# Optimization experiments

Hardware: AMD Instinct MI355X
Metric: run time of the kernel (lower is better)

Reference implementation:

```python
import jax, jax.numpy as jnp
import numpy as np
import math

B, S, D, H, R = 4, 2048, 512, 8, 8  # R = k+1 relative slots per direction


def setup_inputs() -> dict:
    key = jax.random.key(0)
    ks = jax.random.split(key, 16)
    dk = D // H
    sc = 1.0 / math.sqrt(D)
    return {
        "query": jax.random.normal(ks[0], (B, S, D), jnp.float32),
        "key": jax.random.normal(ks[1], (B, S, D), jnp.float32),
        "value": jax.random.normal(ks[2], (B, S, D), jnp.float32),
        "start_nodes": jax.random.randint(ks[3], (B, H, R, S), 0, S, jnp.int64 if jax.config.jax_enable_x64 else jnp.int32),
        "end_nodes": jax.random.randint(ks[4], (B, H, R, S), 0, S, jnp.int64 if jax.config.jax_enable_x64 else jnp.int32),
        "rel_q": jax.random.normal(ks[5], (1, H, 2 * R, dk), jnp.float32),
        "rel_k": jax.random.normal(ks[6], (1, H, 2 * R, dk), jnp.float32),
        "rel_v": jax.random.normal(ks[7], (1, H, 2 * R, dk), jnp.float32),
        "Wq": jax.random.normal(ks[8], (D, D), jnp.float32) * sc,
        "bq": jnp.zeros((D,), jnp.float32),
        "Wk": jax.random.normal(ks[9], (D, D), jnp.float32) * sc,
        "bk": jnp.zeros((D,), jnp.float32),
        "Wv": jax.random.normal(ks[10], (D, D), jnp.float32) * sc,
        "bv": jnp.zeros((D,), jnp.float32),
        "Wo": jax.random.normal(ks[11], (D, D), jnp.float32) * sc,
        "bo": jnp.zeros((D,), jnp.float32),
    }


def reference(query, key, value, start_nodes, end_nodes, rel_q, rel_k, rel_v,
              Wq, bq, Wk, bk, Wv, bv, Wo, bo):
    Bs, Ss, Ds = query.shape
    Hs = start_nodes.shape[1]
    dk = Ds // Hs

    def proj(x, W, b):
        return (x @ W.T + b).reshape(Bs, Ss, Hs, dk).transpose(0, 2, 1, 3)  # [B,H,S,dk]

    q = proj(query, Wq, bq)
    k = proj(key, Wk, bk)
    v = proj(value, Wv, bv)

    start_mask = start_nodes == -1
    sn = jnp.where(start_mask, 0, start_nodes)  # -1 padding -> 0 (masked out below)
    qidx = jnp.concatenate([end_nodes, sn], axis=2)  # [B,H,2R,S]
    kidx = jnp.concatenate([sn, end_nodes], axis=2)

    bi = jnp.arange(Bs)[:, None, None, None]
    hi = jnp.arange(Hs)[None, :, None, None]
    q_ctx = q[bi, hi, qidx]  # [B,H,2R,S,dk]
    k_ctx = k[bi, hi, kidx]
    v_ctx = v[bi, hi, kidx]

    # c2c + c2p + p2c, scale_factor = 3 (rel_q and rel_k both provided)
    scores = ((q_ctx * k_ctx).sum(-1)
              + (q_ctx * rel_k[:, :, :, None, :]).sum(-1)
              + (rel_q[:, :, :, None, :] * k_ctx).sum(-1))
    scores = scores / (3.0 * jnp.sqrt(jnp.asarray(dk, scores.dtype)))

    # mask: padded edges masked in both halves; first S flat entries always masked
    mask = jnp.concatenate([start_mask, start_mask], axis=2).reshape(Bs, Hs, -1)
    mask = mask.at[:, :, :Ss].set(True)
    sflat = jnp.exp(jnp.where(mask, -1e9, scores.reshape(Bs, Hs, -1)))  # [B,H,2R*S]

    qf = qidx.reshape(Bs, Hs, -1)
    b2 = jnp.arange(Bs)[:, None, None]
    h2 = jnp.arange(Hs)[None, :, None]
    # scatter-add softmax denominator over destination nodes, then gather back
    denom = jnp.zeros((Bs, Hs, Ss), sflat.dtype).at[b2, h2, qf].add(sflat)
    denom = jnp.where(denom == 0, -1e9, denom)
    probs = (sflat / denom[b2, h2, qf]).reshape(Bs, Hs, -1, Ss, 1)  # [B,H,2R,S,1]

    attn_v = probs * (v_ctx + rel_v[:, :, :, None, :])  # [B,H,2R,S,dk]
    out = jnp.zeros((Bs, Hs, Ss, dk), attn_v.dtype).at[b2, h2, qf].add(
        attn_v.reshape(Bs, Hs, -1, dk))  # scatter-add aggregation over edges

    out = out.transpose(0, 2, 1, 3).reshape(Bs, Ss, Ds)
    return out @ Wo.T + bo
```

## Files before the change

### kernel.cpp

```cpp
#include <hip/hip_runtime.h>
#include <math.h>

#define B_ 4
#define S_ 2048
#define D_ 512
#define H_ 8
#define R_ 8
#define DK_ 64
#define EPB   (2*R_*S_)
#define ELLCAP 64

typedef __attribute__((ext_vector_type(8))) short bf16x8;
typedef __attribute__((ext_vector_type(8))) unsigned short ushort8_t;
typedef __attribute__((ext_vector_type(4))) float f32x4;

__device__ inline unsigned short f2bf(float f) {
    unsigned u = __builtin_bit_cast(unsigned, f);
    u += 0x7fffu + ((u >> 16) & 1u);
    return (unsigned short)(u >> 16);
}
__device__ inline float bf2f(unsigned short u) {
    return __builtin_bit_cast(float, ((unsigned)u) << 16);
}

__global__ __launch_bounds__(256) void prep(
    const float* __restrict__ query, const float* __restrict__ key,
    const float* __restrict__ value,
    const float* __restrict__ Wq, const float* __restrict__ Wk,
    const float* __restrict__ Wv, const float* __restrict__ Wo,
    const float* __restrict__ rel_q, const float* __restrict__ rel_k,
    const float* __restrict__ rel_v,
    unsigned short* __restrict__ aq, unsigned short* __restrict__ ak,
    unsigned short* __restrict__ av,
    unsigned short* __restrict__ wqp, unsigned short* __restrict__ wkp,
    unsigned short* __restrict__ wvp, unsigned short* __restrict__ wop,
    unsigned short* __restrict__ rqb, unsigned short* __restrict__ rkb,
    unsigned short* __restrict__ rvb)
{
    int bid = blockIdx.x;
    int t = threadIdx.x;
    if (bid < 6656) {
        const float* x;
        unsigned short* y;
        int fi;
        if (bid < 6144) {
            int z = bid >> 11;
            x = (z == 0) ? query : (z == 1) ? key : value;
            y = (z == 0) ? aq : (z == 1) ? ak : av;
            fi = (bid & 2047) * 256 + t;
        } else {
            int r = bid - 6144;
            int z = r >> 7;
            x = (z == 0) ? Wq : (z == 1) ? Wk : (z == 2) ? Wv : Wo;
            y = (z == 0) ? wqp : (z == 1) ? wkp : (z == 2) ? wvp : wop;
            fi = (r & 127) * 256 + t;
        }
        int lane = fi & 63;
        int mg   = fi >> 10;
        int kc   = (fi >> 6) & 15;
        int row  = mg * 16 + (lane & 15);
        int col  = kc * 32 + ((lane >> 4) << 3);
        const float* src = x + (size_t)row * D_ + col;
        float4 a0 = *(const float4*)src;
        float4 a1 = *(const float4*)(src + 4);
        ushort8_t c;
        c[0] = f2bf(a0.x); c[1] = f2bf(a0.y); c[2] = f2bf(a0.z); c[3] = f2bf(a0.w);
        c[4] = f2bf(a1.x); c[5] = f2bf(a1.y); c[6] = f2bf(a1.z); c[7] = f2bf(a1.w);
        *(ushort8_t*)&y[(size_t)fi * 8] = c;
    } else {
        int rr = bid - 6656;
        int z = rr >> 3;
        const float* x = (z == 0) ? rel_q : (z == 1) ? rel_k : rel_v;
        unsigned short* y = (z == 0) ? rqb : (z == 1) ? rkb : rvb;
        size_t i = ((size_t)(rr & 7) * 256 + t) * 4;
        float4 v = *(const float4*)&x[i];
        *(ushort4*)&y[i] = make_ushort4(f2bf(v.x), f2bf(v.y), f2bf(v.z), f2bf(v.w));
    }
}

__global__ __launch_bounds__(256) void gemm_qkv(
    const unsigned short* __restrict__ A0, const unsigned short* __restrict__ A1,
    const unsigned short* __restrict__ A2,
    const unsigned short* __restrict__ W0, const unsigned short* __restrict__ W1,
    const unsigned short* __restrict__ W2,
    const float* __restrict__ bi0, const float* __restrict__ bi1, const float* __restrict__ bi2,
    unsigned short* __restrict__ C0, unsigned short* __restrict__ C1,
    unsigned short* __restrict__ C2)
{
    const int bi  = blockIdx.x;
    const int xcd = bi & 7;
    const int r   = bi >> 3;
    const int z   = r >> 5;
    const int rr  = r & 31;
    const int mg0 = (xcd * 8 + (rr >> 2)) * 8;
    const int ng0 = (rr & 3) * 8;

    const unsigned short* A = (z == 0) ? A0 : (z == 1) ? A1 : A2;
    const unsigned short* W = (z == 0) ? W0 : (z == 1) ? W1 : W2;
    const float* bias       = (z == 0) ? bi0 : (z == 1) ? bi1 : bi2;
    unsigned short* C       = (z == 0) ? C0 : (z == 1) ? C1 : C2;

    const int t    = threadIdx.x;
    const int lane = t & 63;
    const int w    = t >> 6;
    const int wm   = w >> 1, wn = w & 1;

    f32x4 acc[4][4] = {};

    #pragma unroll 2
    for (int kc = 0; kc < 16; ++kc) {
        bf16x8 af[4], bfr[4];
        #pragma unroll
        for (int fm = 0; fm < 4; ++fm) {
            int mg = mg0 + wm * 4 + fm;
            af[fm] = *(const bf16x8*)&A[(size_t)(((mg * 16 + kc) << 6) + lane) * 8];
        }
        #pragma unroll
        for (int fn = 0; fn < 4; ++fn) {
            int ng = ng0 + wn * 4 + fn;
            bfr[fn] = *(const bf16x8*)&W[(size_t)(((ng * 16 + kc) << 6) + lane) * 8];
        }
        #pragma unroll
        for (int fm = 0; fm < 4; ++fm)
            #pragma unroll
            for (int fn = 0; fn < 4; ++fn)
                acc[fm][fn] = __builtin_amdgcn_mfma_f32_16x16x32_bf16(af[fm], bfr[fn], acc[fm][fn], 0, 0, 0);
    }

    #pragma unroll
    for (int fm = 0; fm < 4; ++fm) {
        #pragma unroll
        for (int fn = 0; fn < 4; ++fn) {
            #pragma unroll
            for (int rg = 0; rg < 4; ++rg) {
                int m = (mg0 + wm * 4 + fm) * 16 + (lane >> 4) * 4 + rg;
                int n = (ng0 + wn * 4 + fn) * 16 + (lane & 15);
                float val = acc[fm][fn][rg] + bias[n];
                int b = m >> 11, s = m & (S_ - 1);
                int h = n >> 6,  d = n & 63;
                C[((((size_t)b * H_ + h) * S_ + s) << 6) + d] = f2bf(val);
            }
        }
    }
}

__global__ __launch_bounds__(256) void gemm_out(
    const unsigned short* __restrict__ A, const unsigned short* __restrict__ W,
    const float* __restrict__ bias, float* __restrict__ Cf)
{
    const int bi  = blockIdx.x;
    const int xcd = bi & 7;
    const int r   = bi >> 3;
    const int mg0 = (xcd * 8 + (r >> 3)) * 8;
    const int ng0 = (r & 7) * 4;

    const int t    = threadIdx.x;
    const int lane = t & 63;
    const int w    = t >> 6;
    const int wm   = w >> 1, wn = w & 1;

    f32x4 acc[4][2] = {};

    #pragma unroll 2
    for (int kc = 0; kc < 16; ++kc) {
        bf16x8 af[4], bfr[2];
        #pragma unroll
        for (int fm = 0; fm < 4; ++fm) {
            int mg = mg0 + wm * 4 + fm;
            af[fm] = *(const bf16x8*)&A[(size_t)(((mg * 16 + kc) << 6) + lane) * 8];
        }
        #pragma unroll
        for (int fn = 0; fn < 2; ++fn) {
            int ng = ng0 + wn * 2 + fn;
            bfr[fn] = *(const bf16x8*)&W[(size_t)(((ng * 16 + kc) << 6) + lane) * 8];
        }
        #pragma unroll
        for (int fm = 0; fm < 4; ++fm)
            #pragma unroll
            for (int fn = 0; fn < 2; ++fn)
                acc[fm][fn] = __builtin_amdgcn_mfma_f32_16x16x32_bf16(af[fm], bfr[fn], acc[fm][fn], 0, 0, 0);
    }

    #pragma unroll
    for (int fm = 0; fm < 4; ++fm) {
        #pragma unroll
        for (int fn = 0; fn < 2; ++fn) {
            #pragma unroll
            for (int rg = 0; rg < 4; ++rg) {
                int m = (mg0 + wm * 4 + fm) * 16 + (lane >> 4) * 4 + rg;
                int n = (ng0 + wn * 2 + fn) * 16 + (lane & 15);
                Cf[(size_t)m * D_ + n] = acc[fm][fn][rg] + bias[n];
            }
        }
    }
}

__global__ __launch_bounds__(1024) void attn_fused(
    const unsigned short* __restrict__ q, const unsigned short* __restrict__ k_,
    const unsigned short* __restrict__ v_,
    const unsigned short* __restrict__ rel_q, const unsigned short* __restrict__ rel_k,
    const unsigned short* __restrict__ rel_v,
    const int* __restrict__ start_nodes, const int* __restrict__ end_nodes,
    unsigned short* __restrict__ attn)
{
    __shared__ unsigned short ell[128 * ELLCAP];
    __shared__ int cnt[128];
    const int bi  = blockIdx.x;
    const int xcd = bi & 7;
    const int loc = bi >> 3;
    const int bh  = xcd * 4 + (loc >> 4);
    const int dlo = (loc & 15) << 7;
    const int t   = threadIdx.x;

    if (t < 128) cnt[t] = 0;
    __syncthreads();

    const int base_idx = bh * (R_ * S_);
    for (int f = t; f < EPB; f += 1024) {
        int r2 = f >> 11;
        if (r2 == 0) continue;
        int s = f & (S_ - 1);
        int idx = base_idx + (r2 & 7) * S_ + s;
        int sn = start_nodes[idx];
        if (sn == -1) continue;
        int en = end_nodes[idx];
        int dst = (r2 < R_) ? en : sn;
        unsigned rel = (unsigned)(dst - dlo);
        if (rel < 128u) {
            int ki = (r2 < R_) ? sn : en;
            int pos = atomicAdd(&cnt[rel], 1);
            if (pos < ELLCAP)
                ell[(rel << 6) + pos] = (unsigned short)((r2 << 11) | ki);
        }
    }
    __syncthreads();

    const int w    = t >> 6;
    const int lane = t & 63;
    const int grp  = lane >> 3;
    const int sub  = lane & 7;
    const int h    = bh & 7;
    const size_t node_base = ((size_t)bh << 11);

    for (int dd = 0; dd < 8; ++dd) {
        int dl  = dd * 16 + w;
        int dst = dlo + dl;

        ushort8_t q8 = *(const ushort8_t*)&q[((node_base + dst) << 6) + sub * 8];
        float qv[8];
        #pragma unroll
        for (int i = 0; i < 8; ++i) qv[i] = bf2f(q8[i]);

        int n = cnt[dl];
        if (n > ELLCAP) n = ELLCAP;
        int d_all = (int)ell[(dl << 6) + lane];

        float den = 0.f;
        float o[8] = {};
        #pragma unroll 2
        for (int j = 0; j < n; j += 8) {
            int slot = j + grp;
            int d = __shfl(d_all, slot);
            bool valid = slot < n;
            int ki = d & (S_ - 1);
            int r2 = (d >> 11) & 15;
            ushort8_t k8  = *(const ushort8_t*)&k_  [((node_base + ki) << 6) + sub * 8];
            ushort8_t rk8 = *(const ushort8_t*)&rel_k[(((h << 4) + r2) << 6) + sub * 8];
            ushort8_t rq8 = *(const ushort8_t*)&rel_q[(((h << 4) + r2) << 6) + sub * 8];
            float p = 0.f;
            #pragma unroll
            for (int i = 0; i < 8; ++i)
                p = fmaf(bf2f(k8[i]), qv[i] + bf2f(rq8[i]),
                         fmaf(qv[i], bf2f(rk8[i]), p));
            p += __shfl_xor(p, 1);
            p += __shfl_xor(p, 2);
            p += __shfl_xor(p, 4);
            float sf = valid ? __expf(p * (1.0f / 24.0f)) : 0.f;
            ushort8_t v8  = *(const ushort8_t*)&v_  [((node_base + ki) << 6) + sub * 8];
            ushort8_t rv8 = *(const ushort8_t*)&rel_v[(((h << 4) + r2) << 6) + sub * 8];
            den += sf;
            #pragma unroll
            for (int i = 0; i < 8; ++i)
                o[i] = fmaf(sf, bf2f(v8[i]) + bf2f(rv8[i]), o[i]);
        }
        den += __shfl_xor(den, 8); den += __shfl_xor(den, 16); den += __shfl_xor(den, 32);
        #pragma unroll
        for (int i = 0; i < 8; ++i) {
            o[i] += __shfl_xor(o[i], 8);
            o[i] += __shfl_xor(o[i], 16);
            o[i] += __shfl_xor(o[i], 32);
        }
        if (grp == 0) {
            float inv = (den > 0.f) ? 1.0f / den : 0.f;
            ushort8_t rs;
            #pragma unroll
            for (int i = 0; i < 8; ++i) rs[i] = f2bf(o[i] * inv);
            int m  = ((bh >> 3) << 11) + dst;
            int kc = (h << 1) + (sub >> 2);
            int ln = (m & 15) + ((sub & 3) << 4);
            *(ushort8_t*)&attn[(size_t)((((m >> 4) * 16 + kc) << 6) + ln) * 8] = rs;
        }
    }
}

extern "C" void kernel_launch(void* const* d_in, const int* in_sizes, int n_in,
                              void* d_out, int out_size, void* d_ws, size_t ws_size,
                              hipStream_t stream) {
    const float* query = (const float*)d_in[0];
    const float* key   = (const float*)d_in[1];
    const float* value = (const float*)d_in[2];
    const int* start_nodes = (const int*)d_in[3];
    const int* end_nodes   = (const int*)d_in[4];
    const float* rel_q = (const float*)d_in[5];
    const float* rel_k = (const float*)d_in[6];
    const float* rel_v = (const float*)d_in[7];
    const float* Wq = (const float*)d_in[8];
    const float* bq = (const float*)d_in[9];
    const float* Wk = (const float*)d_in[10];
    const float* bk = (const float*)d_in[11];
    const float* Wv = (const float*)d_in[12];
    const float* bv = (const float*)d_in[13];
    const float* Wo = (const float*)d_in[14];
    const float* bo = (const float*)d_in[15];
    float* out = (float*)d_out;

    const size_t NQ = (size_t)B_ * H_ * S_ * DK_;
    const size_t NW = (size_t)D_ * D_;
    const size_t NR = (size_t)H_ * 2 * R_ * DK_;
    unsigned short* p = (unsigned short*)d_ws;
    unsigned short* aq = p;            p += NQ;
    unsigned short* ak = p;            p += NQ;
    unsigned short* av = p;            p += NQ;
    unsigned short* q  = p;            p += NQ;
    unsigned short* k  = p;            p += NQ;
    unsigned short* v  = p;            p += NQ;
    unsigned short* attn = p;          p += NQ;
    unsigned short* wqp = p;           p += NW;
    unsigned short* wkp = p;           p += NW;
    unsigned short* wvp = p;           p += NW;
    unsigned short* wop = p;           p += NW;
    unsigned short* rqb = p;           p += NR;
    unsigned short* rkb = p;           p += NR;
    unsigned short* rvb = p;           p += NR;

    prep<<<6680, 256, 0, stream>>>(query, key, value, Wq, Wk, Wv, Wo,
                                   rel_q, rel_k, rel_v,
                                   aq, ak, av, wqp, wkp, wvp, wop,
                                   rqb, rkb, rvb);

    gemm_qkv<<<768, 256, 0, stream>>>(aq, ak, av, wqp, wkp, wvp,
                                      bq, bk, bv, q, k, v);

    attn_fused<<<512, 1024, 0, stream>>>(q, k, v, rqb, rkb, rvb,
                                         start_nodes, end_nodes, attn);

    gemm_out<<<512, 256, 0, stream>>>(attn, wop, bo, out);
}
```

Baseline: 226.1 us.

## Fuse fp32-to-bf16 conversion into QKV GEMM with LDS-staged swizzled tiles

```diff
diff --git a/kernel.cpp b/kernel.cpp
--- a/kernel.cpp
+++ b/kernel.cpp
@@ -23,119 +23,130 @@
     return __builtin_bit_cast(float, ((unsigned)u) << 16);
 }
 
-__global__ __launch_bounds__(256) void prep(
-    const float* __restrict__ query, const float* __restrict__ key,
-    const float* __restrict__ value,
-    const float* __restrict__ Wq, const float* __restrict__ Wk,
-    const float* __restrict__ Wv, const float* __restrict__ Wo,
+__global__ __launch_bounds__(256) void gemm_qkv_fused(
+    const float* __restrict__ A0, const float* __restrict__ A1,
+    const float* __restrict__ A2,
+    const float* __restrict__ W0, const float* __restrict__ W1,
+    const float* __restrict__ W2, const float* __restrict__ Wo,
+    const float* __restrict__ bi0, const float* __restrict__ bi1, const float* __restrict__ bi2,
     const float* __restrict__ rel_q, const float* __restrict__ rel_k,
     const float* __restrict__ rel_v,
-    unsigned short* __restrict__ aq, unsigned short* __restrict__ ak,
-    unsigned short* __restrict__ av,
-    unsigned short* __restrict__ wqp, unsigned short* __restrict__ wkp,
-    unsigned short* __restrict__ wvp, unsigned short* __restrict__ wop,
+    unsigned short* __restrict__ C0, unsigned short* __restrict__ C1,
+    unsigned short* __restrict__ C2,
+    unsigned short* __restrict__ wop,
     unsigned short* __restrict__ rqb, unsigned short* __restrict__ rkb,
     unsigned short* __restrict__ rvb)
 {
-    int bid = blockIdx.x;
-    int t = threadIdx.x;
-    if (bid < 6656) {
-        const float* x;
-        unsigned short* y;
-        int fi;
-        if (bid < 6144) {
-            int z = bid >> 11;
-            x = (z == 0) ? query : (z == 1) ? key : value;
-            y = (z == 0) ? aq : (z == 1) ? ak : av;
-            fi = (bid & 2047) * 256 + t;
+    const int bid = blockIdx.x;
+    const int t   = threadIdx.x;
+
+    if (bid >= 768) {
+        if (bid < 792) {
+            int rr = bid - 768;
+            int z = rr >> 3;
+            const float* x = (z == 0) ? rel_q : (z == 1) ? rel_k : rel_v;
+            unsigned short* y = (z == 0) ? rqb : (z == 1) ? rkb : rvb;
+            size_t i = ((size_t)(rr & 7) * 256 + t) * 4;
+            float4 v = *(const float4*)&x[i];
+            *(ushort4*)&y[i] = make_ushort4(f2bf(v.x), f2bf(v.y), f2bf(v.z), f2bf(v.w));
         } else {
-            int r = bid - 6144;
-            int z = r >> 7;
-            x = (z == 0) ? Wq : (z == 1) ? Wk : (z == 2) ? Wv : Wo;
-            y = (z == 0) ? wqp : (z == 1) ? wkp : (z == 2) ? wvp : wop;
-            fi = (r & 127) * 256 + t;
-        }
-        int lane = fi & 63;
-        int mg   = fi >> 10;
-        int kc   = (fi >> 6) & 15;
-        int row  = mg * 16 + (lane & 15);
-        int col  = kc * 32 + ((lane >> 4) << 3);
-        const float* src = x + (size_t)row * D_ + col;
-        float4 a0 = *(const float4*)src;
-        float4 a1 = *(const float4*)(src + 4);
-        ushort8_t c;
-        c[0] = f2bf(a0.x); c[1] = f2bf(a0.y); c[2] = f2bf(a0.z); c[3] = f2bf(a0.w);
-        c[4] = f2bf(a1.x); c[5] = f2bf(a1.y); c[6] = f2bf(a1.z); c[7] = f2bf(a1.w);
-        *(ushort8_t*)&y[(size_t)fi * 8] = c;
-    } else {
-        int rr = bid - 6656;
-        int z = rr >> 3;
-        const float* x = (z == 0) ? rel_q : (z == 1) ? rel_k : rel_v;
-        unsigned short* y = (z == 0) ? rqb : (z == 1) ? rkb : rvb;
-        size_t i = ((size_t)(rr & 7) * 256 + t) * 4;
-        float4 v = *(const float4*)&x[i];
-        *(ushort4*)&y[i] = make_ushort4(f2bf(v.x), f2bf(v.y), f2bf(v.z), f2bf(v.w));
-    }
-}
-
-__global__ __launch_bounds__(256) void gemm_qkv(
-    const unsigned short* __restrict__ A0, const unsigned short* __restrict__ A1,
-    const unsigned short* __restrict__ A2,
-    const unsigned short* __restrict__ W0, const unsigned short* __restrict__ W1,
-    const unsigned short* __restrict__ W2,
-    const float* __restrict__ bi0, const float* __restrict__ bi1, const float* __restrict__ bi2,
-    unsigned short* __restrict__ C0, unsigned short* __restrict__ C1,
-    unsigned short* __restrict__ C2)
-{
-    const int bi  = blockIdx.x;
-    const int xcd = bi & 7;
-    const int r   = bi >> 3;
+            int fi = (bid - 792) * 256 + t;
+            int lane = fi & 63;
+            int ng   = fi >> 10;
+            int kc   = (fi >> 6) & 15;
+            const float* src = Wo + (size_t)(ng * 16 + (lane & 15)) * D_
+                                  + kc * 32 + ((lane >> 4) << 3);
+            float4 a0 = *(const float4*)src;
+            float4 a1 = *(const float4*)(src + 4);
+            ushort8_t c;
+            c[0] = f2bf(a0.x); c[1] = f2bf(a0.y); c[2] = f2bf(a0.z); c[3] = f2bf(a0.w);
+            c[4] = f2bf(a1.x); c[5] = f2bf(a1.y); c[6] = f2bf(a1.z); c[7] = f2bf(a1.w);
+            *(ushort8_t*)&wop[(size_t)fi * 8] = c;
+        }
+        return;
+    }
+
+    __shared__ unsigned short As[128 * 64];
+    __shared__ unsigned short Ws[128 * 64];
+    const int xcd = bid & 7;
+    const int r   = bid >> 3;
     const int z   = r >> 5;
     const int rr  = r & 31;
-    const int mg0 = (xcd * 8 + (rr >> 2)) * 8;
-    const int ng0 = (rr & 3) * 8;
-
-    const unsigned short* A = (z == 0) ? A0 : (z == 1) ? A1 : A2;
-    const unsigned short* W = (z == 0) ? W0 : (z == 1) ? W1 : W2;
-    const float* bias       = (z == 0) ? bi0 : (z == 1) ? bi1 : bi2;
-    unsigned short* C       = (z == 0) ? C0 : (z == 1) ? C1 : C2;
-
-    const int t    = threadIdx.x;
+    const int m0  = (xcd * 8 + (rr >> 2)) * 128;
+    const int n0  = (rr & 3) * 128;
+
+    const float* A    = (z == 0) ? A0 : (z == 1) ? A1 : A2;
+    const float* W    = (z == 0) ? W0 : (z == 1) ? W1 : W2;
+    const float* bias = (z == 0) ? bi0 : (z == 1) ? bi1 : bi2;
+    unsigned short* C = (z == 0) ? C0 : (z == 1) ? C1 : C2;
+
     const int lane = t & 63;
     const int w    = t >> 6;
     const int wm   = w >> 1, wn = w & 1;
+    const int lr    = lane >> 3;
+    const int cglob = (lane & 7) ^ lr;
 
     f32x4 acc[4][4] = {};
 
-    #pragma unroll 2
-    for (int kc = 0; kc < 16; ++kc) {
-        bf16x8 af[4], bfr[4];
-        #pragma unroll
-        for (int fm = 0; fm < 4; ++fm) {
-            int mg = mg0 + wm * 4 + fm;
-            af[fm] = *(const bf16x8*)&A[(size_t)(((mg * 16 + kc) << 6) + lane) * 8];
-        }
-        #pragma unroll
-        for (int fn = 0; fn < 4; ++fn) {
-            int ng = ng0 + wn * 4 + fn;
-            bfr[fn] = *(const bf16x8*)&W[(size_t)(((ng * 16 + kc) << 6) + lane) * 8];
-        }
-        #pragma unroll
-        for (int fm = 0; fm < 4; ++fm)
-            #pragma unroll
-            for (int fn = 0; fn < 4; ++fn)
-                acc[fm][fn] = __builtin_amdgcn_mfma_f32_16x16x32_bf16(af[fm], bfr[fn], acc[fm][fn], 0, 0, 0);
+    for (int kk = 0; kk < D_; kk += 64) {
+        #pragma unroll
+        for (int i = 0; i < 4; ++i) {
+            int rowl = w * 32 + i * 8;
+            {
+                const float* ga = A + (size_t)(m0 + rowl + lr) * D_ + kk + cglob * 8;
+                float4 a0 = *(const float4*)ga;
+                float4 a1 = *(const float4*)(ga + 4);
+                ushort8_t c;
+                c[0] = f2bf(a0.x); c[1] = f2bf(a0.y); c[2] = f2bf(a0.z); c[3] = f2bf(a0.w);
+                c[4] = f2bf(a1.x); c[5] = f2bf(a1.y); c[6] = f2bf(a1.z); c[7] = f2bf(a1.w);
+                *(ushort8_t*)&As[(rowl + lr) * 64 + (lane & 7) * 8] = c;
+            }
+            {
+                const float* gb = W + (size_t)(n0 + rowl + lr) * D_ + kk + cglob * 8;
+                float4 b0 = *(const float4*)gb;
+                float4 b1 = *(const float4*)(gb + 4);
+                ushort8_t c;
+                c[0] = f2bf(b0.x); c[1] = f2bf(b0.y); c[2] = f2bf(b0.z); c[3] = f2bf(b0.w);
+                c[4] = f2bf(b1.x); c[5] = f2bf(b1.y); c[6] = f2bf(b1.z); c[7] = f2bf(b1.w);
+                *(ushort8_t*)&Ws[(rowl + lr) * 64 + (lane & 7) * 8] = c;
+            }
+        }
+        __syncthreads();
+
+        #pragma unroll
+        for (int ks = 0; ks < 64; ks += 32) {
+            const int c0 = ks >> 3;
+            bf16x8 af[4], bfr[4];
+            #pragma unroll
+            for (int mi = 0; mi < 4; ++mi) {
+                int row = wm * 64 + mi * 16 + (lane & 15);
+                int cp  = (c0 + (lane >> 4)) ^ (lane & 7);
+                af[mi] = *(const bf16x8*)&As[row * 64 + cp * 8];
+            }
+            #pragma unroll
+            for (int nj = 0; nj < 4; ++nj) {
+                int row = wn * 64 + nj * 16 + (lane & 15);
+                int cp  = (c0 + (lane >> 4)) ^ (lane & 7);
+                bfr[nj] = *(const bf16x8*)&Ws[row * 64 + cp * 8];
+            }
+            #pragma unroll
+            for (int mi = 0; mi < 4; ++mi)
+                #pragma unroll
+                for (int nj = 0; nj < 4; ++nj)
+                    acc[mi][nj] = __builtin_amdgcn_mfma_f32_16x16x32_bf16(af[mi], bfr[nj], acc[mi][nj], 0, 0, 0);
+        }
+        __syncthreads();
     }
 
     #pragma unroll
-    for (int fm = 0; fm < 4; ++fm) {
-        #pragma unroll
-        for (int fn = 0; fn < 4; ++fn) {
+    for (int mi = 0; mi < 4; ++mi) {
+        #pragma unroll
+        for (int nj = 0; nj < 4; ++nj) {
             #pragma unroll
             for (int rg = 0; rg < 4; ++rg) {
-                int m = (mg0 + wm * 4 + fm) * 16 + (lane >> 4) * 4 + rg;
-                int n = (ng0 + wn * 4 + fn) * 16 + (lane & 15);
-                float val = acc[fm][fn][rg] + bias[n];
+                int m = m0 + wm * 64 + mi * 16 + (lane >> 4) * 4 + rg;
+                int n = n0 + wn * 64 + nj * 16 + (lane & 15);
+                float val = acc[mi][nj][rg] + bias[n];
                 int b = m >> 11, s = m & (S_ - 1);
                 int h = n >> 6,  d = n & 63;
                 C[((((size_t)b * H_ + h) * S_ + s) << 6) + d] = f2bf(val);
@@ -328,28 +339,18 @@
     const size_t NW = (size_t)D_ * D_;
     const size_t NR = (size_t)H_ * 2 * R_ * DK_;
     unsigned short* p = (unsigned short*)d_ws;
-    unsigned short* aq = p;            p += NQ;
-    unsigned short* ak = p;            p += NQ;
-    unsigned short* av = p;            p += NQ;
-    unsigned short* q  = p;            p += NQ;
-    unsigned short* k  = p;            p += NQ;
-    unsigned short* v  = p;            p += NQ;
+    unsigned short* q    = p;          p += NQ;
+    unsigned short* k    = p;          p += NQ;
+    unsigned short* v    = p;          p += NQ;
     unsigned short* attn = p;          p += NQ;
-    unsigned short* wqp = p;           p += NW;
-    unsigned short* wkp = p;           p += NW;
-    unsigned short* wvp = p;           p += NW;
-    unsigned short* wop = p;           p += NW;
-    unsigned short* rqb = p;           p += NR;
-    unsigned short* rkb = p;           p += NR;
-    unsigned short* rvb = p;           p += NR;
-
-    prep<<<6680, 256, 0, stream>>>(query, key, value, Wq, Wk, Wv, Wo,
-                                   rel_q, rel_k, rel_v,
-                                   aq, ak, av, wqp, wkp, wvp, wop,
-                                   rqb, rkb, rvb);
-
-    gemm_qkv<<<768, 256, 0, stream>>>(aq, ak, av, wqp, wkp, wvp,
-                                      bq, bk, bv, q, k, v);
+    unsigned short* wop  = p;          p += NW;
+    unsigned short* rqb  = p;          p += NR;
+    unsigned short* rkb  = p;          p += NR;
+    unsigned short* rvb  = p;          p += NR;
+
+    gemm_qkv_fused<<<920, 256, 0, stream>>>(
+        query, key, value, Wq, Wk, Wv, Wo, bq, bk, bv,
+        rel_q, rel_k, rel_v, q, k, v, wop, rqb, rkb, rvb);
 
     attn_fused<<<512, 1024, 0, stream>>>(q, k, v, rqb, rkb, rvb,
                                          start_nodes, end_nodes, attn);
```

New measurement: 222.9 us. No clear change (-1.4%).
